# Performance work log

Measured on AMD Instinct MI355X. Metric: run time of the kernel, lower is better.

## Reference

```python
import jax, jax.numpy as jnp
import numpy as np

NEG = -1e30  # finite stand-in for -inf (safe for grads)


def setup_inputs() -> dict:
    key = jax.random.key(0)
    k1, k2, k3 = jax.random.split(key, 3)
    B, T, C, L = 128, 128, 6625, 25
    predicts = jax.random.normal(k1, (B, T, C), dtype=jnp.float32)
    labels = jax.random.randint(k2, (B, L), 1, C, dtype=jnp.int32)  # blank=0 excluded
    label_lengths = jax.random.randint(k3, (B,), 1, L + 1, dtype=jnp.int32)
    return {"predicts": predicts, "labels": labels, "label_lengths": label_lengths}


def _ctc_loss(log_probs, labels, label_lengths):
    # log_probs: [T, B, C]; labels: [B, L]; full input lengths = T (as in original module)
    T, B, C = log_probs.shape
    L = labels.shape[1]
    S = 2 * L + 1  # extended label sequence: blank interleaved, blank=0
    ext = jnp.zeros((B, S), dtype=labels.dtype).at[:, 1::2].set(labels)
    # emission log-probs gathered at extended labels: [T, B, S]
    emit = jnp.take_along_axis(log_probs, jnp.broadcast_to(ext[None, :, :], (T, B, S)), axis=2)
    # skip (s-2 -> s) allowed only when ext[s] != ext[s-2] (blanks never skip)
    skip = jnp.concatenate([jnp.zeros((B, 2), dtype=bool), ext[:, 2:] != ext[:, :-2]], axis=1)

    alpha0 = jnp.full((B, S), NEG, dtype=log_probs.dtype)
    alpha0 = alpha0.at[:, 0].set(emit[0, :, 0]).at[:, 1].set(emit[0, :, 1])

    pad1 = jnp.full((B, 1), NEG, dtype=log_probs.dtype)
    pad2 = jnp.full((B, 2), NEG, dtype=log_probs.dtype)

    def step(alpha, emit_t):
        a1 = jnp.concatenate([pad1, alpha[:, :-1]], axis=1)
        a2 = jnp.where(skip, jnp.concatenate([pad2, alpha[:, :-2]], axis=1), NEG)
        m = jnp.maximum(jnp.maximum(alpha, a1), a2)
        new = m + jnp.log(jnp.exp(alpha - m) + jnp.exp(a1 - m) + jnp.exp(a2 - m)) + emit_t
        return new, None

    alphaT, _ = jax.lax.scan(step, alpha0, emit[1:])
    idx_last = (2 * label_lengths)[:, None]  # final blank position
    ll = jnp.logaddexp(
        jnp.take_along_axis(alphaT, idx_last, axis=1)[:, 0],
        jnp.take_along_axis(alphaT, idx_last - 1, axis=1)[:, 0],
    )
    loss = -ll
    loss = jnp.where(loss > 1e29, 0.0, loss)  # zero_infinity=True
    # reduction='mean': per-sample loss divided by target length, then batch mean
    return jnp.mean(loss / label_lengths.astype(loss.dtype))


def reference(predicts, labels, label_lengths):
    B = predicts.shape[0]
    log_probs = jax.nn.log_softmax(jnp.transpose(predicts, (1, 0, 2)), axis=-1)  # [T,B,C]
    loss = _ctc_loss(log_probs, labels, label_lengths) / B  # module divides again by B
    return loss
```

## Files before the change

kernel.cpp:

```cpp
#include <hip/hip_runtime.h>
#include <math.h>
#include <stdint.h>


#define NEGV (-1e30f)

constexpr int Bc = 128;
constexpr int Tc = 128;
constexpr int Cc = 6625;
constexpr int Lc = 25;
constexpr int Sc = 2 * Lc + 1;
constexpr int VPT = 7;

__global__ __launch_bounds__(256) void k_emit(const float* __restrict__ predicts,
                                              const int* __restrict__ labels,
                                              float* __restrict__ emit,
                                              float* __restrict__ out) {
    const int row = blockIdx.x;
    const int b = row >> 7;
    const float* __restrict__ x = predicts + (size_t)row * Cc;
    const int tid = threadIdx.x;

    if (row == 0 && tid == 0) out[0] = 0.f;

    const int mis = (int)(((uintptr_t)x >> 2) & 3);
    const int npro = (4 - mis) & 3;
    const int nvec = (Cc - npro) >> 2;
    const int ntail = (Cc - npro) & 3;
    const float4* __restrict__ xv = (const float4*)(x + npro);
    const int tbase = npro + (nvec << 2);

    float ssum = 0.f;
    if (tid < npro) ssum += __expf(x[tid]);
    if (tid < ntail) ssum += __expf(x[tbase + tid]);
#pragma unroll
    for (int k = 0; k < VPT; ++k) {
        int j = tid + (k << 8);
        if (j < nvec) {
            float4 v = xv[j];
            ssum += __expf(v.x) + __expf(v.y) + __expf(v.z) + __expf(v.w);
        }
    }
    for (int off = 32; off; off >>= 1) ssum += __shfl_xor(ssum, off);

    __shared__ float sh[4];
    __shared__ float bc;
    const int wave = tid >> 6, lane = tid & 63;
    if (lane == 0) sh[wave] = ssum;
    __syncthreads();
    if (tid == 0) bc = __logf(sh[0] + sh[1] + sh[2] + sh[3]);
    __syncthreads();
    const float lse = bc;

    if (tid < Sc) {
        int c = (tid & 1) ? labels[b * Lc + (tid >> 1)] : 0;
        emit[(size_t)row * Sc + tid] = x[c] - lse;
    }
}

__global__ __launch_bounds__(64) void k_ctc(const float* __restrict__ emit,
                                            const int* __restrict__ labels,
                                            const int* __restrict__ lens,
                                            float* __restrict__ out) {
    const int b = blockIdx.x;
    const int s = threadIdx.x;

    const int ext = (s < Sc && (s & 1)) ? labels[b * Lc + (s >> 1)] : 0;
    const int ext_m2 = __shfl_up(ext, 2);
    const bool skip = (s >= 2) && (s < Sc) && (ext != ext_m2);

    const float* __restrict__ eb = emit + (size_t)b * Tc * Sc;

    float alpha = NEGV;
    if (s == 0) alpha = eb[0];
    else if (s == 1) alpha = eb[1];

    float e = (s < Sc) ? eb[Sc + s] : NEGV;
    for (int t = 1; t < Tc; ++t) {
        float e_next = (t + 1 < Tc && s < Sc) ? eb[(t + 1) * Sc + s] : NEGV;
        float a1 = __shfl_up(alpha, 1);
        if (s < 1) a1 = NEGV;
        float a2 = __shfl_up(alpha, 2);
        if (!skip) a2 = NEGV;
        float m = fmaxf(fmaxf(alpha, a1), a2);
        alpha = m + __logf(__expf(alpha - m) + __expf(a1 - m) + __expf(a2 - m)) + e;
        e = e_next;
    }

    const int len = lens[b];
    const int idx = 2 * len;
    const float ahi = __shfl(alpha, idx);
    const float alo = __shfl(alpha, idx - 1);
    if (s == 0) {
        float mm = fmaxf(ahi, alo);
        float ll = mm + __logf(__expf(ahi - mm) + __expf(alo - mm));
        float loss = -ll;
        if (loss > 1e29f) loss = 0.f;
        atomicAdd(out, loss / ((float)len * (float)Bc * (float)Bc));
    }
}

extern "C" void kernel_launch(void* const* d_in, const int* in_sizes, int n_in,
                              void* d_out, int out_size, void* d_ws, size_t ws_size,
                              hipStream_t stream) {
    const float* predicts = (const float*)d_in[0];
    const int* labels = (const int*)d_in[1];
    const int* lens = (const int*)d_in[2];
    float* out = (float*)d_out;
    float* emit = (float*)d_ws;

    k_emit<<<Bc * Tc, 256, 0, stream>>>(predicts, labels, emit, out);
    k_ctc<<<Bc, 64, 0, stream>>>(emit, labels, lens, out);
}
```

Before: 583.3 us.

## Map one softmax row per wave and prefetch emissions 8 steps ahead in CTC

The emit kernel now gives each 64-lane wave its own row (four rows per block) instead of a whole block per row. This removes the shared-memory reduction and both block barriers, and the label gather is issued early. The CTC recursion is unrolled by 8 with a register-based prefetch of the next 8 emission rows, to hide global load latency in the serial time loop. Each lane now does more sequential loads per row, and register pressure rises.

```diff
diff --git a/kernel.cpp b/kernel.cpp
--- a/kernel.cpp
+++ b/kernel.cpp
@@ -10,52 +10,51 @@
 constexpr int Cc = 6625;
 constexpr int Lc = 25;
 constexpr int Sc = 2 * Lc + 1;
-constexpr int VPT = 7;
 
 __global__ __launch_bounds__(256) void k_emit(const float* __restrict__ predicts,
                                               const int* __restrict__ labels,
                                               float* __restrict__ emit,
                                               float* __restrict__ out) {
-    const int row = blockIdx.x;
+    if (blockIdx.x == 0 && threadIdx.x == 0) out[0] = 0.f;
+
+    const int row = (blockIdx.x << 2) + (threadIdx.x >> 6);
+    const int lane = threadIdx.x & 63;
     const int b = row >> 7;
     const float* __restrict__ x = predicts + (size_t)row * Cc;
-    const int tid = threadIdx.x;
 
-    if (row == 0 && tid == 0) out[0] = 0.f;
+    int c = 0;
+    if (lane < Sc && (lane & 1)) c = labels[b * Lc + (lane >> 1)];
+    float xc = 0.f;
+    if (lane < Sc) xc = x[c];
 
     const int mis = (int)(((uintptr_t)x >> 2) & 3);
     const int npro = (4 - mis) & 3;
     const int nvec = (Cc - npro) >> 2;
     const int ntail = (Cc - npro) & 3;
     const float4* __restrict__ xv = (const float4*)(x + npro);
-    const int tbase = npro + (nvec << 2);
 
     float ssum = 0.f;
-    if (tid < npro) ssum += __expf(x[tid]);
-    if (tid < ntail) ssum += __expf(x[tbase + tid]);
-#pragma unroll
-    for (int k = 0; k < VPT; ++k) {
-        int j = tid + (k << 8);
+    if (lane < npro) ssum += __expf(x[lane]);
+    if (lane < ntail) ssum += __expf(x[npro + (nvec << 2) + lane]);
+
+#pragma unroll 5
+    for (int k = 0; k < 25; ++k) {
+        float4 v = xv[lane + (k << 6)];
+        ssum += __expf(v.x) + __expf(v.y) + __expf(v.z) + __expf(v.w);
+    }
+    {
+        int j = lane + 1600;
         if (j < nvec) {
             float4 v = xv[j];
             ssum += __expf(v.x) + __expf(v.y) + __expf(v.z) + __expf(v.w);
         }
     }
+
+#pragma unroll
     for (int off = 32; off; off >>= 1) ssum += __shfl_xor(ssum, off);
+    const float lse = __logf(ssum);
 
-    __shared__ float sh[4];
-    __shared__ float bc;
-    const int wave = tid >> 6, lane = tid & 63;
-    if (lane == 0) sh[wave] = ssum;
-    __syncthreads();
-    if (tid == 0) bc = __logf(sh[0] + sh[1] + sh[2] + sh[3]);
-    __syncthreads();
-    const float lse = bc;
-
-    if (tid < Sc) {
-        int c = (tid & 1) ? labels[b * Lc + (tid >> 1)] : 0;
-        emit[(size_t)row * Sc + tid] = x[c] - lse;
-    }
+    if (lane < Sc) emit[(size_t)row * Sc + lane] = xc - lse;
 }
 
 __global__ __launch_bounds__(64) void k_ctc(const float* __restrict__ emit,
@@ -70,22 +69,37 @@
     const bool skip = (s >= 2) && (s < Sc) && (ext != ext_m2);
 
     const float* __restrict__ eb = emit + (size_t)b * Tc * Sc;
+    const bool act = (s < Sc);
 
     float alpha = NEGV;
     if (s == 0) alpha = eb[0];
     else if (s == 1) alpha = eb[1];
 
-    float e = (s < Sc) ? eb[Sc + s] : NEGV;
-    for (int t = 1; t < Tc; ++t) {
-        float e_next = (t + 1 < Tc && s < Sc) ? eb[(t + 1) * Sc + s] : NEGV;
-        float a1 = __shfl_up(alpha, 1);
-        if (s < 1) a1 = NEGV;
-        float a2 = __shfl_up(alpha, 2);
-        if (!skip) a2 = NEGV;
-        float m = fmaxf(fmaxf(alpha, a1), a2);
-        alpha = m + __logf(__expf(alpha - m) + __expf(a1 - m) + __expf(a2 - m)) + e;
-        e = e_next;
+#define LD(t) (act ? eb[((t) > Tc - 1 ? Tc - 1 : (t)) * Sc + s] : NEGV)
+#define STEP(EV) do {                                                        \
+        float a1 = __shfl_up(alpha, 1); if (s == 0) a1 = NEGV;               \
+        float a2 = __shfl_up(alpha, 2); if (!skip) a2 = NEGV;                \
+        float m = fmaxf(fmaxf(alpha, a1), a2);                               \
+        alpha = m + __logf(__expf(alpha - m) + __expf(a1 - m) +              \
+                           __expf(a2 - m)) + (EV);                           \
+    } while (0)
+
+    float p0 = LD(1), p1 = LD(2), p2 = LD(3), p3 = LD(4);
+    float p4 = LD(5), p5 = LD(6), p6 = LD(7), p7 = LD(8);
+
+    int tb = 1;
+    for (; tb + 7 < Tc; tb += 8) {
+        float q0 = LD(tb + 8),  q1 = LD(tb + 9),  q2 = LD(tb + 10), q3 = LD(tb + 11);
+        float q4 = LD(tb + 12), q5 = LD(tb + 13), q6 = LD(tb + 14), q7 = LD(tb + 15);
+        STEP(p0); STEP(p1); STEP(p2); STEP(p3);
+        STEP(p4); STEP(p5); STEP(p6); STEP(p7);
+        p0 = q0; p1 = q1; p2 = q2; p3 = q3;
+        p4 = q4; p5 = q5; p6 = q6; p7 = q7;
     }
+    STEP(p0); STEP(p1); STEP(p2); STEP(p3); STEP(p4); STEP(p5); STEP(p6);
+
+#undef LD
+#undef STEP
 
     const int len = lens[b];
     const int idx = 2 * len;
@@ -109,6 +123,6 @@
     float* out = (float*)d_out;
     float* emit = (float*)d_ws;
 
-    k_emit<<<Bc * Tc, 256, 0, stream>>>(predicts, labels, emit, out);
+    k_emit<<<(Bc * Tc) / 4, 256, 0, stream>>>(predicts, labels, emit, out);
     k_ctc<<<Bc, 64, 0, stream>>>(emit, labels, lens, out);
 }
```

Result: no change. 577.6 us (-1.0%).
